# Kernel optimization log

Hardware: AMD Instinct MI355X
Metric: run time of the kernel (lower is better)

The kernel has to match this reference:

```python
import jax, jax.numpy as jnp
import numpy as np

N = 100000   # num_nodes_total
E = 1600000  # num edges (avg degree 16)
ES = 30000   # scored triples
R = 16       # num_relations
D = 128      # cfg.dim


def setup_inputs() -> dict:
    key = jax.random.key(0)
    ks = jax.random.split(key, 10)
    x0 = 0.01 * jax.random.normal(ks[0], (N, D), dtype=jnp.float32)  # Embedding init std=0.01
    # GCNConv lin: Glorot init, no bias in lin; separate zero bias added post-aggregation
    glorot = np.sqrt(6.0 / (D + D)).astype(np.float32)
    W1 = jax.random.uniform(ks[1], (D, D), jnp.float32, -glorot, glorot)
    b1 = jnp.zeros((D,), jnp.float32)
    W2 = jax.random.uniform(ks[2], (D, D), jnp.float32, -glorot, glorot)
    b2 = jnp.zeros((D,), jnp.float32)
    rel_W = jax.random.uniform(ks[3], (R, D, D), jnp.float32, -glorot, glorot)  # xavier_uniform
    edge_index = jax.random.randint(ks[4], (2, E), 0, N)
    rel_ids = jax.random.randint(ks[5], (ES,), 0, R)
    head = jax.random.randint(ks[6], (ES,), 0, N)
    tail = jax.random.randint(ks[7], (ES,), 0, N)
    return {"x0": x0, "W1": W1, "b1": b1, "W2": W2, "b2": b2,
            "rel_W": rel_W, "edge_index": edge_index, "rel_ids": rel_ids,
            "head": head, "tail": tail}


def _gcn_conv(x, W, b, src, dst, norm):
    # GCNConv(add_self_loops=False, normalize=True): out = scatter(norm * (xW)[src] -> dst) + b
    h = x @ W                           # (N, D)
    msg = h[src] * norm[:, None]        # (E, D)
    return jax.ops.segment_sum(msg, dst, num_segments=x.shape[0]) + b


def reference(x0, W1, b1, W2, b2, rel_W, edge_index, rel_ids, head, tail):
    src, dst = edge_index[0], edge_index[1]
    n = x0.shape[0]
    # symmetric gcn_norm without self-loops: deg over targets, norm = d^-1/2[src]*d^-1/2[dst]
    deg = jax.ops.segment_sum(jnp.ones_like(src, dtype=x0.dtype), dst, num_segments=n)
    dinv = jnp.where(deg > 0, 1.0 / jnp.sqrt(jnp.maximum(deg, 1.0)), 0.0)
    norm = dinv[src] * dinv[dst]
    # encode (eval mode: dropout is identity)
    x = jax.nn.relu(_gcn_conv(x0, W1, b1, src, dst, norm))
    z = _gcn_conv(x, W2, b2, src, dst, norm)
    # score_logits_all_rel: z[head]^T W[rel] z[tail]
    scores = jnp.einsum('ed,edf,ef->e', z[head], rel_W[rel_ids], z[tail])
    return scores
```

## Files before the change

### kernel.cpp

```cpp
#include <hip/hip_runtime.h>
#include <hip/hip_bf16.h>

#define TD 128
#define WS 136
#define SC_T 8
#define BKT_SH 7
#define NBLK 256

typedef __attribute__((ext_vector_type(8))) short bf16x8;
typedef __attribute__((ext_vector_type(4))) float f32x4;

static __device__ __forceinline__ unsigned short f2bf(float f) {
    unsigned int u = __float_as_uint(f);
    u += 0x7fffu + ((u >> 16) & 1u);
    return (unsigned short)(u >> 16);
}
static __device__ __forceinline__ float bf2f(unsigned short h) {
    return __uint_as_float((unsigned int)h << 16);
}


__global__ __launch_bounds__(256) void kc_hist(const int* __restrict__ ei, int* __restrict__ bh,
                                               const int* __restrict__ rel, int* __restrict__ rcount,
                                               int E_, int ES_, int NB, int chunk, int rchunk) {
    __shared__ int lh[1024];
    __shared__ int rh[16];
    int t = threadIdx.x, blk = blockIdx.x;
    for (int j = t; j < NB; j += 256) lh[j] = 0;
    if (t < 16) rh[t] = 0;
    __syncthreads();
    int e0 = blk * chunk, e1 = min(E_, e0 + chunk);
    for (int e = e0 + t; e < e1; e += 256)
        atomicAdd(&lh[ei[E_ + e] >> BKT_SH], 1);
    int r0 = blk * rchunk, r1 = min(ES_, r0 + rchunk);
    for (int e = r0 + t; e < r1; e += 256)
        atomicAdd(&rh[rel[e]], 1);
    __syncthreads();
    for (int j = t; j < NB; j += 256) bh[(size_t)j * NBLK + blk] = lh[j];
    if (t < 16 && rh[t]) atomicAdd(&rcount[t], rh[t]);
}

__global__ __launch_bounds__(64) void kc_scanA(int* __restrict__ bh, int* __restrict__ tot, int NB) {
    int b = blockIdx.x, l = threadIdx.x;
    int* row = bh + (size_t)b * NBLK;
    int run = 0;
#pragma unroll
    for (int g = 0; g < NBLK / 64; ++g) {
        int v = row[g * 64 + l];
        int x = v;
#pragma unroll
        for (int off = 1; off < 64; off <<= 1) {
            int y = __shfl_up(x, off);
            if (l >= off) x += y;
        }
        row[g * 64 + l] = run + x - v;
        run += __shfl(x, 63);
    }
    if (l == 0) tot[b] = run;
}

__global__ __launch_bounds__(256) void kc_scanB(const int* __restrict__ tot, int* __restrict__ boff,
                                                int NB, int* __restrict__ rowptrN) {
    __shared__ int wsum[4];
    int t = threadIdx.x;
    int base = t * 4;
    int a0 = (base     < NB) ? tot[base]     : 0;
    int a1 = (base + 1 < NB) ? tot[base + 1] : 0;
    int a2 = (base + 2 < NB) ? tot[base + 2] : 0;
    int a3 = (base + 3 < NB) ? tot[base + 3] : 0;
    int s1 = a0 + a1, s2 = s1 + a2, tt = s2 + a3;
    int lane = t & 63, wv = t >> 6;
    int x = tt;
#pragma unroll
    for (int off = 1; off < 64; off <<= 1) {
        int y = __shfl_up(x, off);
        if (lane >= off) x += y;
    }
    if (lane == 63) wsum[wv] = x;
    __syncthreads();
    int woff = 0;
    for (int w = 0; w < wv; ++w) woff += wsum[w];
    int excl = woff + x - tt;
    if (base     < NB) boff[base]     = excl;
    if (base + 1 < NB) boff[base + 1] = excl + a0;
    if (base + 2 < NB) boff[base + 2] = excl + s1;
    if (base + 3 < NB) boff[base + 3] = excl + s2;
    if (t == 255) { boff[NB] = woff + x; *rowptrN = woff + x; }
}

__global__ __launch_bounds__(256) void kc_scat(const int* __restrict__ ei, const int* __restrict__ bh,
                                               const int* __restrict__ boff, int* __restrict__ ebuf,
                                               int E_, int NB, int chunk) {
    __shared__ int lh[1024];
    int t = threadIdx.x, blk = blockIdx.x;
    for (int j = t; j < NB; j += 256) lh[j] = 0;
    __syncthreads();
    int e0 = blk * chunk, e1 = min(E_, e0 + chunk);
    for (int e = e0 + t; e < e1; e += 256) {
        int s = ei[e];
        int d = ei[E_ + e];
        int b = d >> BKT_SH;
        int lr = atomicAdd(&lh[b], 1);
        int slot = boff[b] + bh[(size_t)b * NBLK + blk] + lr;
        ebuf[slot] = (s << BKT_SH) | (d & ((1 << BKT_SH) - 1));
    }
}

__global__ __launch_bounds__(256) void kc_build(const int* __restrict__ ebuf, const int* __restrict__ boff,
                                                int* __restrict__ rowptr, float* __restrict__ dinv,
                                                int* __restrict__ esrc, int n) {
    __shared__ int hist[128], excl[128], cur[128];
    __shared__ int w0;
    int b = blockIdx.x, t = threadIdx.x;
    int node0 = b << BKT_SH;
    int s = boff[b], e = boff[b + 1];
    if (t < 128) { hist[t] = 0; cur[t] = 0; }
    __syncthreads();
    for (int i = s + t; i < e; i += 256)
        atomicAdd(&hist[ebuf[i] & 127], 1);
    __syncthreads();
    int v = (t < 128) ? hist[t] : 0;
    int lane = t & 63, wv = t >> 6;
    int x = v;
#pragma unroll
    for (int off = 1; off < 64; off <<= 1) {
        int y = __shfl_up(x, off);
        if (lane >= off) x += y;
    }
    if (t == 63) w0 = x;
    __syncthreads();
    if (t < 128) {
        int ex = x - v + (wv == 1 ? w0 : 0);
        excl[t] = ex;
        int node = node0 + t;
        if (node < n) {
            rowptr[node] = s + ex;
            dinv[node] = (v > 0) ? 1.0f / sqrtf((float)v) : 0.0f;
        }
    }
    __syncthreads();
    for (int i = s + t; i < e; i += 256) {
        int p = ebuf[i];
        int loc = p & 127;
        int lr = atomicAdd(&cur[loc], 1);
        esrc[s + excl[loc] + lr] = p >> BKT_SH;
    }
}

__global__ __launch_bounds__(256) void k_wsplit(const float* __restrict__ W1, const float* __restrict__ W2,
                                                unsigned short* __restrict__ Wt) {
    int i = blockIdx.x * 256 + threadIdx.x;
    int w = i >> 14;
    int idx = i & 16383;
    int k = idx >> 7, n = idx & 127;
    float x = (w ? W2 : W1)[idx];
    unsigned short h = f2bf(x);
    unsigned short l = f2bf(x - bf2f(h));
    size_t base = (size_t)w * 32768;
    Wt[base + n * 128 + k] = h;
    Wt[base + 16384 + n * 128 + k] = l;
}

__global__ __launch_bounds__(256, 2) void k_gemm(const float* __restrict__ X,
                                                 const unsigned short* __restrict__ Wth,
                                                 const unsigned short* __restrict__ Wtl,
                                                 const float* __restrict__ scale,
                                                 unsigned char* __restrict__ out8,
                                                 float* __restrict__ scOut,
                                                 int nrows) {
    __shared__ __align__(16) unsigned short Wl[2][128 * WS];
    const int t = threadIdx.x;
    const int w = t >> 6;
    const int lane = t & 63;
    const int l15 = lane & 15;
    const int quad = lane >> 4;
    const int rbase = blockIdx.x * 64 + w * 16;
    const int arow = rbase + l15;
    const bool avalid = arow < nrows;

    float4 xa[4][2];
#pragma unroll
    for (int kc = 0; kc < 4; ++kc) {
        const float* src = X + (size_t)arow * TD + kc * 32 + quad * 8;
        xa[kc][0] = avalid ? *(const float4*)src       : make_float4(0.f, 0.f, 0.f, 0.f);
        xa[kc][1] = avalid ? *(const float4*)(src + 4) : make_float4(0.f, 0.f, 0.f, 0.f);
    }

    {
        const uint4* gh = (const uint4*)Wth;
        const uint4* gl = (const uint4*)Wtl;
#pragma unroll
        for (int it = 0; it < 8; ++it) {
            int idx = t + it * 256;
            int n = idx >> 4, kg = idx & 15;
            uint4 vh = gh[idx];
            uint4 vl = gl[idx];
            *(uint4*)&Wl[0][n * WS + kg * 8] = vh;
            *(uint4*)&Wl[1][n * WS + kg * 8] = vl;
        }
    }

    bf16x8 ah[4], al[4];
#pragma unroll
    for (int kc = 0; kc < 4; ++kc) {
#pragma unroll
        for (int j = 0; j < 8; ++j) {
            float v = (j < 4) ? ((const float*)&xa[kc][0])[j] : ((const float*)&xa[kc][1])[j - 4];
            unsigned short h = f2bf(v);
            ah[kc][j] = (short)h;
            al[kc][j] = (short)f2bf(v - bf2f(h));
        }
    }
    __syncthreads();

    f32x4 acc[8];
#pragma unroll
    for (int b = 0; b < 8; ++b) acc[b] = (f32x4){0.f, 0.f, 0.f, 0.f};

#pragma unroll
    for (int kc = 0; kc < 4; ++kc) {
        const int koff = kc * 32 + quad * 8;
#pragma unroll
        for (int b = 0; b < 8; ++b) {
            const int boff = (b * 16 + l15) * WS + koff;
            bf16x8 bh = *(const bf16x8*)&Wl[0][boff];
            bf16x8 bl = *(const bf16x8*)&Wl[1][boff];
            acc[b] = __builtin_amdgcn_mfma_f32_16x16x32_bf16(ah[kc], bh, acc[b], 0, 0, 0);
            acc[b] = __builtin_amdgcn_mfma_f32_16x16x32_bf16(al[kc], bh, acc[b], 0, 0, 0);
            acc[b] = __builtin_amdgcn_mfma_f32_16x16x32_bf16(ah[kc], bl, acc[b], 0, 0, 0);
        }
    }

    __syncthreads();

    {
        unsigned char* lds8 = (unsigned char*)&Wl[0][0];
        const int grow = rbase + quad * 4;
        float4 s4 = make_float4(0.f, 0.f, 0.f, 0.f);
        if (grow < nrows) s4 = *(const float4*)&scale[grow];
        float rm[4];
#pragma unroll
        for (int j = 0; j < 4; ++j) {
            float sj = ((const float*)&s4)[j];
            float mx = 0.f;
#pragma unroll
            for (int b = 0; b < 8; ++b) {
                acc[b][j] *= sj;
                mx = fmaxf(mx, fabsf(acc[b][j]));
            }
            rm[j] = mx;
        }
#pragma unroll
        for (int m_ = 1; m_ < 16; m_ <<= 1)
#pragma unroll
            for (int j = 0; j < 4; ++j) rm[j] = fmaxf(rm[j], __shfl_xor(rm[j], m_));
        float inv[4];
#pragma unroll
        for (int j = 0; j < 4; ++j) inv[j] = rm[j] > 0.f ? 127.f / rm[j] : 0.f;
#pragma unroll
        for (int j = 0; j < 4; ++j) {
            int lrow = w * 16 + quad * 4 + j;
#pragma unroll
            for (int b = 0; b < 8; ++b) {
                int q = (int)rintf(acc[b][j] * inv[j]);
                lds8[lrow * 128 + b * 16 + l15] = (unsigned char)(signed char)q;
            }
        }
        if (l15 == 0 && grow < nrows)
            *(float4*)&scOut[grow] = make_float4(rm[0] * (1.f / 127.f), rm[1] * (1.f / 127.f),
                                                 rm[2] * (1.f / 127.f), rm[3] * (1.f / 127.f));
    }
    __syncthreads();
    {
        const unsigned int* lds32 = (const unsigned int*)&Wl[0][0];
        unsigned int* g32 = (unsigned int*)out8;
#pragma unroll
        for (int k = 0; k < 8; ++k) {
            int idx = t + k * 256;
            int row = blockIdx.x * 64 + (idx >> 5);
            if (row < nrows) g32[(size_t)blockIdx.x * 2048 + idx] = lds32[idx];
        }
    }
}

#define ACCI8(p, u, s) \
    p##0 = fmaf(s, (float)(signed char)(u.x      ), p##0); \
    p##1 = fmaf(s, (float)(signed char)(u.x >>  8), p##1); \
    p##2 = fmaf(s, (float)(signed char)(u.x >> 16), p##2); \
    p##3 = fmaf(s, (float)(signed char)(u.x >> 24), p##3); \
    p##4 = fmaf(s, (float)(signed char)(u.y      ), p##4); \
    p##5 = fmaf(s, (float)(signed char)(u.y >>  8), p##5); \
    p##6 = fmaf(s, (float)(signed char)(u.y >> 16), p##6); \
    p##7 = fmaf(s, (float)(signed char)(u.y >> 24), p##7);

__global__ __launch_bounds__(256) void k_agg(const unsigned char* __restrict__ hs8, const float* __restrict__ sc,
                                             const int* __restrict__ rowptr, const int* __restrict__ esrc,
                                             const float* __restrict__ dinv, const float* __restrict__ bias,
                                             float* __restrict__ out, int n, int relu) {
    int node = blockIdx.x * 16 + (threadIdx.x >> 4);
    int lane = threadIdx.x & 15;
    if (node >= n) return;
    int s = rowptr[node], e = rowptr[node + 1];
    const uint2* h8 = (const uint2*)hs8;
    float a0 = 0.f, a1 = 0.f, a2 = 0.f, a3 = 0.f, a4 = 0.f, a5 = 0.f, a6 = 0.f, a7 = 0.f;
    float c0 = 0.f, c1 = 0.f, c2 = 0.f, c3 = 0.f, c4 = 0.f, c5 = 0.f, c6 = 0.f, c7 = 0.f;
    int i = s;
    for (; i + 4 <= e; i += 4) {
        int s0 = esrc[i], s1 = esrc[i + 1], s2 = esrc[i + 2], s3 = esrc[i + 3];
        uint2 u0 = h8[(size_t)s0 * 16 + lane];
        uint2 u1 = h8[(size_t)s1 * 16 + lane];
        uint2 u2 = h8[(size_t)s2 * 16 + lane];
        uint2 u3 = h8[(size_t)s3 * 16 + lane];
        float f0 = sc[s0], f1 = sc[s1], f2 = sc[s2], f3 = sc[s3];
        ACCI8(a, u0, f0)
        ACCI8(c, u1, f1)
        ACCI8(a, u2, f2)
        ACCI8(c, u3, f3)
    }
    for (; i < e; ++i) {
        int s0 = esrc[i];
        uint2 u = h8[(size_t)s0 * 16 + lane];
        float f = sc[s0];
        ACCI8(a, u, f)
    }
    a0 += c0; a1 += c1; a2 += c2; a3 += c3;
    a4 += c4; a5 += c5; a6 += c6; a7 += c7;
    float di = dinv[node];
    float4 b0 = ((const float4*)bias)[lane * 2];
    float4 b1 = ((const float4*)bias)[lane * 2 + 1];
    float o0 = fmaf(di, a0, b0.x);
    float o1 = fmaf(di, a1, b0.y);
    float o2 = fmaf(di, a2, b0.z);
    float o3 = fmaf(di, a3, b0.w);
    float o4 = fmaf(di, a4, b1.x);
    float o5 = fmaf(di, a5, b1.y);
    float o6 = fmaf(di, a6, b1.z);
    float o7 = fmaf(di, a7, b1.w);
    if (relu) {
        o0 = fmaxf(o0, 0.f); o1 = fmaxf(o1, 0.f); o2 = fmaxf(o2, 0.f); o3 = fmaxf(o3, 0.f);
        o4 = fmaxf(o4, 0.f); o5 = fmaxf(o5, 0.f); o6 = fmaxf(o6, 0.f); o7 = fmaxf(o7, 0.f);
    }
    ((float4*)out)[(size_t)node * 32 + lane * 2]     = make_float4(o0, o1, o2, o3);
    ((float4*)out)[(size_t)node * 32 + lane * 2 + 1] = make_float4(o4, o5, o6, o7);
}

__global__ void k_roff(const int* __restrict__ rcount, int* __restrict__ roff,
                       int* __restrict__ chunkoff, int* __restrict__ cursor, int nr) {
    if (threadIdx.x == 0 && blockIdx.x == 0) {
        int run = 0, crun = 0;
        for (int r = 0; r < nr; ++r) {
            roff[r] = run; chunkoff[r] = crun; cursor[r] = run;
            run += rcount[r]; crun += (rcount[r] + SC_T - 1) / SC_T;
        }
        roff[nr] = run; chunkoff[nr] = crun;
    }
}

__global__ __launch_bounds__(256) void k_bucket(const int* __restrict__ rel, int* __restrict__ cursor,
                                                int* __restrict__ eidx, int es) {
    __shared__ int lh[16];
    __shared__ int lbase[16];
    int t = threadIdx.x;
    if (t < 16) lh[t] = 0;
    __syncthreads();
    int r[4], lr[4];
#pragma unroll
    for (int i = 0; i < 4; ++i) {
        int e = blockIdx.x * 1024 + i * 256 + t;
        if (e < es) {
            r[i] = rel[e];
            lr[i] = atomicAdd(&lh[r[i]], 1);
        } else r[i] = -1;
    }
    __syncthreads();
    if (t < 16) lbase[t] = lh[t] ? atomicAdd(&cursor[t], lh[t]) : 0;
    __syncthreads();
#pragma unroll
    for (int i = 0; i < 4; ++i)
        if (r[i] >= 0) eidx[lbase[r[i]] + lr[i]] = blockIdx.x * 1024 + i * 256 + t;
}

__global__ __launch_bounds__(256) void k_score_r(const float* __restrict__ z, const float* __restrict__ relW,
                                                 const int* __restrict__ eidx, const int* __restrict__ head,
                                                 const int* __restrict__ tail, const int* __restrict__ roff,
                                                 const int* __restrict__ chunkoff, float* __restrict__ out,
                                                 int R_, int cpb) {
    __shared__ __align__(16) float Wl[TD * TD];
    __shared__ __align__(16) float zhL[SC_T * TD];
    __shared__ __align__(16) float ztL[SC_T * TD];
    __shared__ int eids[SC_T];
    __shared__ int co[17], ro[17];
    __shared__ float red[4][SC_T];
    const int t = threadIdx.x;
    if (t < 17 && t <= R_) { co[t] = chunkoff[t]; ro[t] = roff[t]; }
    __syncthreads();
    const int nch = co[R_];
    int b = blockIdx.x * cpb;
    const int bend = min(nch, b + cpb);
    int r = 0, rprev = -1;
    for (; b < bend; ++b) {
        while (co[r + 1] <= b) ++r;
        const int base = ro[r] + (b - co[r]) * SC_T;
        const int nt = min(SC_T, ro[r + 1] - base);
        if (t < SC_T) eids[t] = (t < nt) ? eidx[base + t] : -1;
        const bool newW = (r != rprev);
        rprev = r;
        __syncthreads();
        {
            int tt = t >> 5, c4 = t & 31;
            float4 vh = make_float4(0.f, 0.f, 0.f, 0.f), vt = vh;
            int e = eids[tt];
            if (e >= 0) {
                vh = ((const float4*)(z + (size_t)head[e] * TD))[c4];
                vt = ((const float4*)(z + (size_t)tail[e] * TD))[c4];
            }
            ((float4*)(zhL + tt * TD))[c4] = vh;
            ((float4*)(ztL + tt * TD))[c4] = vt;
        }
        if (newW) {
            const float4* W4 = (const float4*)(relW + (size_t)r * TD * TD);
            float4* Wl4 = (float4*)Wl;
#pragma unroll
            for (int i = 0; i < 16; ++i) Wl4[t + i * 256] = W4[t + i * 256];
        }
        __syncthreads();

        const int c  = (t & 31) * 4;
        const int i0 = (t >> 5) * 16;
        float4 acc[SC_T];
#pragma unroll
        for (int u = 0; u < SC_T; ++u) acc[u] = make_float4(0.f, 0.f, 0.f, 0.f);
#pragma unroll 4
        for (int i = i0; i < i0 + 16; ++i) {
            float4 wv = *(const float4*)&Wl[i * TD + c];
#pragma unroll
            for (int u = 0; u < SC_T; ++u) {
                float h = zhL[u * TD + i];
                acc[u].x = fmaf(h, wv.x, acc[u].x);
                acc[u].y = fmaf(h, wv.y, acc[u].y);
                acc[u].z = fmaf(h, wv.z, acc[u].z);
                acc[u].w = fmaf(h, wv.w, acc[u].w);
            }
        }
        float pth[SC_T];
#pragma unroll
        for (int u = 0; u < SC_T; ++u) {
            float4 z4 = *(const float4*)&ztL[u * TD + c];
            pth[u] = acc[u].x * z4.x + acc[u].y * z4.y + acc[u].z * z4.z + acc[u].w * z4.w;
        }
#pragma unroll
        for (int off = 32; off > 0; off >>= 1)
#pragma unroll
            for (int u = 0; u < SC_T; ++u) pth[u] += __shfl_down(pth[u], off);
        if ((t & 63) == 0) {
            int wv = t >> 6;
#pragma unroll
            for (int u = 0; u < SC_T; ++u) red[wv][u] = pth[u];
        }
        __syncthreads();
        if (t < SC_T) {
            int e = eids[t];
            if (e >= 0) out[e] = red[0][t] + red[1][t] + red[2][t] + red[3][t];
        }
    }
}

extern "C" void kernel_launch(void* const* d_in, const int* in_sizes, int n_in,
                              void* d_out, int out_size, void* d_ws, size_t ws_size,
                              hipStream_t stream) {
    const float* x0   = (const float*)d_in[0];
    const float* W1   = (const float*)d_in[1];
    const float* b1   = (const float*)d_in[2];
    const float* W2   = (const float*)d_in[3];
    const float* b2   = (const float*)d_in[4];
    const float* relW = (const float*)d_in[5];
    const int*   ei   = (const int*)d_in[6];
    const int*   rel  = (const int*)d_in[7];
    const int*   head = (const int*)d_in[8];
    const int*   tail = (const int*)d_in[9];
    float* outp = (float*)d_out;

    const int N_  = in_sizes[0] / TD;
    const int E_  = in_sizes[6] / 2;
    const int ES_ = in_sizes[7];
    const int R_  = in_sizes[5] / (TD * TD);
    const int ntiles64 = (N_ + 63) / 64;
    const int NB    = (N_ + (1 << BKT_SH) - 1) >> BKT_SH;
    const int chunk  = (E_ + NBLK - 1) / NBLK;
    const int rchunk = (ES_ + NBLK - 1) / NBLK;
    const int maxch  = (ES_ + SC_T - 1) / SC_T + R_;
    const int sgrid  = maxch < 512 ? maxch : 512;
    const int cpb    = (maxch + sgrid - 1) / sgrid;

    char* p = (char*)d_ws;
    auto alloc = [&](size_t bytes) { char* r = p; p += (bytes + 255) & ~(size_t)255; return r; };
    float*          dinv   = (float*)         alloc((size_t)N_ * 4);
    int*            rowptr = (int*)           alloc(((size_t)N_ + 1) * 4);
    int*            bh     = (int*)           alloc((size_t)NB * NBLK * 4);
    int*            tot    = (int*)           alloc((size_t)NB * 4);
    int*            boff   = (int*)           alloc(((size_t)NB + 1) * 4);
    int*            esrc   = (int*)           alloc((size_t)E_ * 4);
    unsigned short* Wt     = (unsigned short*)alloc((size_t)4 * 16384 * 2);
    int*            rcount = (int*)           alloc((size_t)R_ * 4);
    int*            roff   = (int*)           alloc(((size_t)R_ + 1) * 4);
    int*            chkoff = (int*)           alloc(((size_t)R_ + 1) * 4);
    int*            cursor = (int*)           alloc((size_t)R_ * 4);
    int*            eidx   = (int*)           alloc((size_t)ES_ * 4);
    unsigned char*  bufA   = (unsigned char*) alloc((size_t)N_ * TD);
    float*          sc     = (float*)         alloc((size_t)N_ * 4);
    float*          bufB   = (float*)         alloc((size_t)N_ * TD * 4);
    int*            ebuf   = (int*)bufA;

    hipMemsetAsync(rcount, 0, (size_t)R_ * 4, stream);

    kc_hist <<<NBLK, 256, 0, stream>>>(ei, bh, rel, rcount, E_, ES_, NB, chunk, rchunk);
    kc_scanA<<<NB, 64, 0, stream>>>(bh, tot, NB);
    kc_scanB<<<1, 256, 0, stream>>>(tot, boff, NB, rowptr + N_);
    kc_scat <<<NBLK, 256, 0, stream>>>(ei, bh, boff, ebuf, E_, NB, chunk);
    kc_build<<<NB, 256, 0, stream>>>(ebuf, boff, rowptr, dinv, esrc, N_);

    k_wsplit<<<128, 256, 0, stream>>>(W1, W2, Wt);

    k_roff  <<<1, 64, 0, stream>>>(rcount, roff, chkoff, cursor, R_);
    k_bucket<<<(ES_ + 1023) / 1024, 256, 0, stream>>>(rel, cursor, eidx, ES_);

    k_gemm<<<ntiles64, 256, 0, stream>>>(x0, Wt, Wt + 16384, dinv, bufA, sc, N_);
    k_agg <<<(N_ + 15) / 16, 256, 0, stream>>>(bufA, sc, rowptr, esrc, dinv, b1, bufB, N_, 1);
    k_gemm<<<ntiles64, 256, 0, stream>>>(bufB, Wt + 32768, Wt + 49152, dinv, bufA, sc, N_);
    k_agg <<<(N_ + 15) / 16, 256, 0, stream>>>(bufA, sc, rowptr, esrc, dinv, b2, bufB, N_, 0);

    k_score_r<<<sgrid, 256, 0, stream>>>(bufB, relW, eidx, head, tail,
                                         roff, chkoff, outp, R_, cpb);
}
```

Before: 326.1 us.

## Drop split-bf16 GEMM, fuse setup kernels, and double-buffer relation scoring

```diff
diff --git a/kernel.cpp b/kernel.cpp
--- a/kernel.cpp
+++ b/kernel.cpp
@@ -22,10 +22,19 @@
 
 __global__ __launch_bounds__(256) void kc_hist(const int* __restrict__ ei, int* __restrict__ bh,
                                                const int* __restrict__ rel, int* __restrict__ rcount,
+                                               const float* __restrict__ W1, const float* __restrict__ W2,
+                                               unsigned short* __restrict__ Wt,
                                                int E_, int ES_, int NB, int chunk, int rchunk) {
     __shared__ int lh[1024];
     __shared__ int rh[16];
     int t = threadIdx.x, blk = blockIdx.x;
+    if (blk >= NBLK) {
+        int idx = (blk - NBLK) * 256 + t;
+        int k = idx >> 7, n = idx & 127;
+        Wt[n * 128 + k] = f2bf(W1[idx]);
+        Wt[16384 + n * 128 + k] = f2bf(W2[idx]);
+        return;
+    }
     for (int j = t; j < NB; j += 256) lh[j] = 0;
     if (t < 16) rh[t] = 0;
     __syncthreads();
@@ -60,7 +69,9 @@
 }
 
 __global__ __launch_bounds__(256) void kc_scanB(const int* __restrict__ tot, int* __restrict__ boff,
-                                                int NB, int* __restrict__ rowptrN) {
+                                                int NB, int* __restrict__ rowptrN,
+                                                const int* __restrict__ rcount, int* __restrict__ roff,
+                                                int* __restrict__ chunkoff, int* __restrict__ cursor, int nr) {
     __shared__ int wsum[4];
     int t = threadIdx.x;
     int base = t * 4;
@@ -86,6 +97,14 @@
     if (base + 2 < NB) boff[base + 2] = excl + s1;
     if (base + 3 < NB) boff[base + 3] = excl + s2;
     if (t == 255) { boff[NB] = woff + x; *rowptrN = woff + x; }
+    if (t == 0) {
+        int run = 0, crun = 0;
+        for (int r = 0; r < nr; ++r) {
+            roff[r] = run; chunkoff[r] = crun; cursor[r] = run;
+            run += rcount[r]; crun += (rcount[r] + SC_T - 1) / SC_T;
+        }
+        roff[nr] = run; chunkoff[nr] = crun;
+    }
 }
 
 __global__ __launch_bounds__(256) void kc_scat(const int* __restrict__ ei, const int* __restrict__ bh,
@@ -147,28 +166,13 @@
     }
 }
 
-__global__ __launch_bounds__(256) void k_wsplit(const float* __restrict__ W1, const float* __restrict__ W2,
-                                                unsigned short* __restrict__ Wt) {
-    int i = blockIdx.x * 256 + threadIdx.x;
-    int w = i >> 14;
-    int idx = i & 16383;
-    int k = idx >> 7, n = idx & 127;
-    float x = (w ? W2 : W1)[idx];
-    unsigned short h = f2bf(x);
-    unsigned short l = f2bf(x - bf2f(h));
-    size_t base = (size_t)w * 32768;
-    Wt[base + n * 128 + k] = h;
-    Wt[base + 16384 + n * 128 + k] = l;
-}
-
-__global__ __launch_bounds__(256, 2) void k_gemm(const float* __restrict__ X,
+__global__ __launch_bounds__(256, 4) void k_gemm(const float* __restrict__ X,
                                                  const unsigned short* __restrict__ Wth,
-                                                 const unsigned short* __restrict__ Wtl,
                                                  const float* __restrict__ scale,
                                                  unsigned char* __restrict__ out8,
                                                  float* __restrict__ scOut,
                                                  int nrows) {
-    __shared__ __align__(16) unsigned short Wl[2][128 * WS];
+    __shared__ __align__(16) unsigned short Wl[128 * WS];
     const int t = threadIdx.x;
     const int w = t >> 6;
     const int lane = t & 63;
@@ -188,27 +192,22 @@
 
     {
         const uint4* gh = (const uint4*)Wth;
-        const uint4* gl = (const uint4*)Wtl;
 #pragma unroll
         for (int it = 0; it < 8; ++it) {
             int idx = t + it * 256;
             int n = idx >> 4, kg = idx & 15;
             uint4 vh = gh[idx];
-            uint4 vl = gl[idx];
-            *(uint4*)&Wl[0][n * WS + kg * 8] = vh;
-            *(uint4*)&Wl[1][n * WS + kg * 8] = vl;
-        }
-    }
-
-    bf16x8 ah[4], al[4];
+            *(uint4*)&Wl[n * WS + kg * 8] = vh;
+        }
+    }
+
+    bf16x8 ah[4];
 #pragma unroll
     for (int kc = 0; kc < 4; ++kc) {
 #pragma unroll
         for (int j = 0; j < 8; ++j) {
             float v = (j < 4) ? ((const float*)&xa[kc][0])[j] : ((const float*)&xa[kc][1])[j - 4];
-            unsigned short h = f2bf(v);
-            ah[kc][j] = (short)h;
-            al[kc][j] = (short)f2bf(v - bf2f(h));
+            ah[kc][j] = (short)f2bf(v);
         }
     }
     __syncthreads();
@@ -222,19 +221,15 @@
         const int koff = kc * 32 + quad * 8;
 #pragma unroll
         for (int b = 0; b < 8; ++b) {
-            const int boff = (b * 16 + l15) * WS + koff;
-            bf16x8 bh = *(const bf16x8*)&Wl[0][boff];
-            bf16x8 bl = *(const bf16x8*)&Wl[1][boff];
+            bf16x8 bh = *(const bf16x8*)&Wl[(b * 16 + l15) * WS + koff];
             acc[b] = __builtin_amdgcn_mfma_f32_16x16x32_bf16(ah[kc], bh, acc[b], 0, 0, 0);
-            acc[b] = __builtin_amdgcn_mfma_f32_16x16x32_bf16(al[kc], bh, acc[b], 0, 0, 0);
-            acc[b] = __builtin_amdgcn_mfma_f32_16x16x32_bf16(ah[kc], bl, acc[b], 0, 0, 0);
         }
     }
 
     __syncthreads();
 
     {
-        unsigned char* lds8 = (unsigned char*)&Wl[0][0];
+        unsigned char* lds8 = (unsigned char*)&Wl[0];
         const int grow = rbase + quad * 4;
         float4 s4 = make_float4(0.f, 0.f, 0.f, 0.f);
         if (grow < nrows) s4 = *(const float4*)&scale[grow];
@@ -272,7 +267,7 @@
     }
     __syncthreads();
     {
-        const unsigned int* lds32 = (const unsigned int*)&Wl[0][0];
+        const unsigned int* lds32 = (const unsigned int*)&Wl[0];
         unsigned int* g32 = (unsigned int*)out8;
 #pragma unroll
         for (int k = 0; k < 8; ++k) {
@@ -344,18 +339,6 @@
     ((float4*)out)[(size_t)node * 32 + lane * 2 + 1] = make_float4(o4, o5, o6, o7);
 }
 
-__global__ void k_roff(const int* __restrict__ rcount, int* __restrict__ roff,
-                       int* __restrict__ chunkoff, int* __restrict__ cursor, int nr) {
-    if (threadIdx.x == 0 && blockIdx.x == 0) {
-        int run = 0, crun = 0;
-        for (int r = 0; r < nr; ++r) {
-            roff[r] = run; chunkoff[r] = crun; cursor[r] = run;
-            run += rcount[r]; crun += (rcount[r] + SC_T - 1) / SC_T;
-        }
-        roff[nr] = run; chunkoff[nr] = crun;
-    }
-}
-
 __global__ __launch_bounds__(256) void k_bucket(const int* __restrict__ rel, int* __restrict__ cursor,
                                                 int* __restrict__ eidx, int es) {
     __shared__ int lh[16];
@@ -386,56 +369,64 @@
                                                  const int* __restrict__ chunkoff, float* __restrict__ out,
                                                  int R_, int cpb) {
     __shared__ __align__(16) float Wl[TD * TD];
-    __shared__ __align__(16) float zhL[SC_T * TD];
-    __shared__ __align__(16) float ztL[SC_T * TD];
-    __shared__ int eids[SC_T];
-    __shared__ int co[17], ro[17];
-    __shared__ float red[4][SC_T];
+    __shared__ __align__(16) float zhL[2][SC_T * TD];
+    __shared__ int eids[2][SC_T];
+    __shared__ float red[2][4][SC_T];
     const int t = threadIdx.x;
-    if (t < 17 && t <= R_) { co[t] = chunkoff[t]; ro[t] = roff[t]; }
-    __syncthreads();
-    const int nch = co[R_];
-    int b = blockIdx.x * cpb;
-    const int bend = min(nch, b + cpb);
-    int r = 0, rprev = -1;
-    for (; b < bend; ++b) {
-        while (co[r + 1] <= b) ++r;
-        const int base = ro[r] + (b - co[r]) * SC_T;
-        const int nt = min(SC_T, ro[r + 1] - base);
-        if (t < SC_T) eids[t] = (t < nt) ? eidx[base + t] : -1;
-        const bool newW = (r != rprev);
-        rprev = r;
-        __syncthreads();
-        {
-            int tt = t >> 5, c4 = t & 31;
-            float4 vh = make_float4(0.f, 0.f, 0.f, 0.f), vt = vh;
-            int e = eids[tt];
-            if (e >= 0) {
-                vh = ((const float4*)(z + (size_t)head[e] * TD))[c4];
-                vt = ((const float4*)(z + (size_t)tail[e] * TD))[c4];
-            }
-            ((float4*)(zhL + tt * TD))[c4] = vh;
-            ((float4*)(ztL + tt * TD))[c4] = vt;
-        }
-        if (newW) {
-            const float4* W4 = (const float4*)(relW + (size_t)r * TD * TD);
-            float4* Wl4 = (float4*)Wl;
-#pragma unroll
-            for (int i = 0; i < 16; ++i) Wl4[t + i * 256] = W4[t + i * 256];
-        }
-        __syncthreads();
-
-        const int c  = (t & 31) * 4;
-        const int i0 = (t >> 5) * 16;
+    const int nch = chunkoff[R_];
+    int b0 = (int)blockIdx.x * cpb;
+    const int bend = min(nch, b0 + cpb);
+    if (b0 >= bend) return;
+
+    auto stage_z = [&](int b, int rr, int buf) {
+        int base = roff[rr] + (b - chunkoff[rr]) * SC_T;
+        int nt2 = min(SC_T, roff[rr + 1] - base);
+        int tt = t >> 5, c4 = t & 31;
+        if (t < SC_T) eids[buf][t] = (t < nt2) ? eidx[base + t] : -1;
+        int e = (tt < nt2) ? eidx[base + tt] : -1;
+        float4 vh = make_float4(0.f, 0.f, 0.f, 0.f);
+        if (e >= 0) vh = ((const float4*)(z + (size_t)head[e] * TD))[c4];
+        ((float4*)(zhL[buf] + tt * TD))[c4] = vh;
+    };
+    auto stage_W = [&](int rr) {
+        const float4* W4 = (const float4*)(relW + (size_t)rr * TD * TD);
+        float4* Wl4 = (float4*)Wl;
+#pragma unroll
+        for (int i = 0; i < 16; ++i) Wl4[t + i * 256] = W4[t + i * 256];
+    };
+
+    int r = 0;
+    while (chunkoff[r + 1] <= b0) ++r;
+    stage_z(b0, r, 0);
+    stage_W(r);
+    __syncthreads();
+    int cur = 0;
+    const int c  = (t & 31) * 4;
+    const int i0 = (t >> 5) * 16;
+    for (int b = b0; b < bend; ++b) {
+        int rn = r;
+        const bool havenext = (b + 1 < bend);
+        if (havenext) while (chunkoff[rn + 1] <= b + 1) ++rn;
+        const bool sameW = havenext && (rn == r);
+        if (sameW) stage_z(b + 1, rn, cur ^ 1);
+
+        float4 ztr[SC_T];
+#pragma unroll
+        for (int u = 0; u < SC_T; ++u) {
+            int e = eids[cur][u];
+            ztr[u] = make_float4(0.f, 0.f, 0.f, 0.f);
+            if (e >= 0) ztr[u] = *(const float4*)(z + (size_t)tail[e] * TD + c);
+        }
         float4 acc[SC_T];
 #pragma unroll
         for (int u = 0; u < SC_T; ++u) acc[u] = make_float4(0.f, 0.f, 0.f, 0.f);
+        const float* zh = zhL[cur];
 #pragma unroll 4
         for (int i = i0; i < i0 + 16; ++i) {
             float4 wv = *(const float4*)&Wl[i * TD + c];
 #pragma unroll
             for (int u = 0; u < SC_T; ++u) {
-                float h = zhL[u * TD + i];
+                float h = zh[u * TD + i];
                 acc[u].x = fmaf(h, wv.x, acc[u].x);
                 acc[u].y = fmaf(h, wv.y, acc[u].y);
                 acc[u].z = fmaf(h, wv.z, acc[u].z);
@@ -444,24 +435,28 @@
         }
         float pth[SC_T];
 #pragma unroll
-        for (int u = 0; u < SC_T; ++u) {
-            float4 z4 = *(const float4*)&ztL[u * TD + c];
-            pth[u] = acc[u].x * z4.x + acc[u].y * z4.y + acc[u].z * z4.z + acc[u].w * z4.w;
-        }
+        for (int u = 0; u < SC_T; ++u)
+            pth[u] = acc[u].x * ztr[u].x + acc[u].y * ztr[u].y + acc[u].z * ztr[u].z + acc[u].w * ztr[u].w;
 #pragma unroll
         for (int off = 32; off > 0; off >>= 1)
 #pragma unroll
             for (int u = 0; u < SC_T; ++u) pth[u] += __shfl_down(pth[u], off);
         if ((t & 63) == 0) {
-            int wv = t >> 6;
-#pragma unroll
-            for (int u = 0; u < SC_T; ++u) red[wv][u] = pth[u];
+            int wv2 = t >> 6;
+#pragma unroll
+            for (int u = 0; u < SC_T; ++u) red[cur][wv2][u] = pth[u];
         }
         __syncthreads();
         if (t < SC_T) {
-            int e = eids[t];
-            if (e >= 0) out[e] = red[0][t] + red[1][t] + red[2][t] + red[3][t];
-        }
+            int e = eids[cur][t];
+            if (e >= 0) out[e] = red[cur][0][t] + red[cur][1][t] + red[cur][2][t] + red[cur][3][t];
+        }
+        if (havenext && !sameW) {
+            stage_z(b + 1, rn, cur ^ 1);
+            stage_W(rn);
+            __syncthreads();
+        }
+        r = rn; cur ^= 1;
     }
 }
 
@@ -500,7 +495,7 @@
     int*            tot    = (int*)           alloc((size_t)NB * 4);
     int*            boff   = (int*)           alloc(((size_t)NB + 1) * 4);
     int*            esrc   = (int*)           alloc((size_t)E_ * 4);
-    unsigned short* Wt     = (unsigned short*)alloc((size_t)4 * 16384 * 2);
+    unsigned short* Wt     = (unsigned short*)alloc((size_t)2 * 16384 * 2);
     int*            rcount = (int*)           alloc((size_t)R_ * 4);
     int*            roff   = (int*)           alloc(((size_t)R_ + 1) * 4);
     int*            chkoff = (int*)           alloc(((size_t)R_ + 1) * 4);
@@ -513,20 +508,17 @@
 
     hipMemsetAsync(rcount, 0, (size_t)R_ * 4, stream);
 
-    kc_hist <<<NBLK, 256, 0, stream>>>(ei, bh, rel, rcount, E_, ES_, NB, chunk, rchunk);
+    kc_hist <<<NBLK + 64, 256, 0, stream>>>(ei, bh, rel, rcount, W1, W2, Wt, E_, ES_, NB, chunk, rchunk);
     kc_scanA<<<NB, 64, 0, stream>>>(bh, tot, NB);
-    kc_scanB<<<1, 256, 0, stream>>>(tot, boff, NB, rowptr + N_);
+    kc_scanB<<<1, 256, 0, stream>>>(tot, boff, NB, rowptr + N_, rcount, roff, chkoff, cursor, R_);
     kc_scat <<<NBLK, 256, 0, stream>>>(ei, bh, boff, ebuf, E_, NB, chunk);
     kc_build<<<NB, 256, 0, stream>>>(ebuf, boff, rowptr, dinv, esrc, N_);
 
-    k_wsplit<<<128, 256, 0, stream>>>(W1, W2, Wt);
-
-    k_roff  <<<1, 64, 0, stream>>>(rcount, roff, chkoff, cursor, R_);
     k_bucket<<<(ES_ + 1023) / 1024, 256, 0, stream>>>(rel, cursor, eidx, ES_);
 
-    k_gemm<<<ntiles64, 256, 0, stream>>>(x0, Wt, Wt + 16384, dinv, bufA, sc, N_);
+    k_gemm<<<ntiles64, 256, 0, stream>>>(x0, Wt, dinv, bufA, sc, N_);
     k_agg <<<(N_ + 15) / 16, 256, 0, stream>>>(bufA, sc, rowptr, esrc, dinv, b1, bufB, N_, 1);
-    k_gemm<<<ntiles64, 256, 0, stream>>>(bufB, Wt + 32768, Wt + 49152, dinv, bufA, sc, N_);
+    k_gemm<<<ntiles64, 256, 0, stream>>>(bufB, Wt + 16384, dinv, bufA, sc, N_);
     k_agg <<<(N_ + 15) / 16, 256, 0, stream>>>(bufA, sc, rowptr, esrc, dinv, b2, bufB, N_, 0);
 
     k_score_r<<<sgrid, 256, 0, stream>>>(bufB, relW, eidx, head, tail,
```

Measured after the change: 330.6 us. About the same (+1.4%).
